# Optimization experiments

Measured on AMD Instinct MI355X. Metric: run time of the kernel, lower is better.

The kernel has to match this reference:

```python
import jax, jax.numpy as jnp
import numpy as np

B, C, H, W = 4, 2048, 14, 14
N_CLS, WORD_D, INT_D = 80, 300, 1024


def setup_inputs() -> dict:
    key = jax.random.key(0)
    ks = jax.random.split(key, 8)
    s = lambda fan_in: 1.0 / np.sqrt(fan_in)
    return {
        "img_feature_map": jax.random.normal(ks[0], (B, C, H, W), jnp.float32),
        "word_features": jax.random.normal(ks[1], (N_CLS, WORD_D), jnp.float32),
        "fc1_w": jax.random.uniform(ks[2], (INT_D, C), jnp.float32, -s(C), s(C)),
        "fc2_w": jax.random.uniform(ks[3], (INT_D, WORD_D), jnp.float32, -s(WORD_D), s(WORD_D)),
        "fc3_w": jax.random.uniform(ks[4], (INT_D, INT_D), jnp.float32, -s(INT_D), s(INT_D)),
        "fc3_b": jax.random.uniform(ks[5], (INT_D,), jnp.float32, -s(INT_D), s(INT_D)),
        "fc4_w": jax.random.uniform(ks[6], (1, INT_D), jnp.float32, -s(INT_D), s(INT_D)),
        "fc4_b": jax.random.uniform(ks[7], (1,), jnp.float32, -s(INT_D), s(INT_D)),
    }


def reference(img_feature_map, word_features, fc1_w, fc2_w, fc3_w, fc3_b, fc4_w, fc4_b):
    b, c, h, w = img_feature_map.shape
    n = word_features.shape[0]
    # [B,C,H,W] -> [B,H,W,C]
    x = jnp.transpose(img_feature_map, (0, 2, 3, 1))
    img_p = jnp.einsum('bhwc,dc->bhwd', x, fc1_w)            # [B,H,W,INT_D]
    word_p = word_features @ fc2_w.T                          # [N,INT_D]
    # broadcast product instead of .repeat(): [B,H,W,N,INT_D]
    feat = jnp.tanh(img_p[:, :, :, None, :] * word_p[None, None, None, :, :])
    feat = jnp.einsum('bhwnd,ed->bhwne', feat, fc3_w) + fc3_b
    coef = jnp.einsum('bhwnd,d->bhwn', feat, fc4_w[0]) + fc4_b[0]  # [B,H,W,N]
    # softmax over spatial positions per (batch, class)
    coef = jax.nn.softmax(coef.reshape(b, h * w, n), axis=1).reshape(b, h, w, n)
    # weighted spatial pooling: [B,N,C]
    return jnp.einsum('bhwn,bhwc->bnc', coef, x)
```

## Files before the change

kernel.cpp:

```cpp
#include <hip/hip_runtime.h>

typedef __attribute__((ext_vector_type(8))) short short8;
typedef __attribute__((ext_vector_type(4))) float f32x4;
typedef __attribute__((ext_vector_type(4))) unsigned short u16x4;

#define B_   4
#define C_   2048
#define HW_  196
#define P_   784
#define NCLS 80
#define WD   300
#define ID   1024

#define WP_OFF    0
#define V_OFF     81920
#define BS_OFF    82944
#define IMGP_OFF  83968
#define LG_OFF    3295232
#define VPART_OFF 3357952
#define ABF_BYTE  13748224
#define WBF_BYTE  16959488

__device__ __forceinline__ unsigned short f2bf(float x) {
    unsigned u = __float_as_uint(x);
    return (unsigned short)((u + 0x7FFFu + ((u >> 16) & 1u)) >> 16);
}

__global__ __launch_bounds__(256) void k_prep(const float* __restrict__ img,
                                              const float* __restrict__ wf,
                                              const float* __restrict__ fc1w,
                                              const float* __restrict__ fc2w,
                                              const float* __restrict__ fc3w,
                                              const float* __restrict__ fc4w,
                                              unsigned short* __restrict__ abf,
                                              unsigned short* __restrict__ wbf,
                                              float* __restrict__ wp,
                                              float* __restrict__ vpart) {
    __shared__ unsigned short tile[HW_][68];
    int bid = blockIdx.x, t = threadIdx.x;
    if (bid < 320) {
        int idx = bid * 256 + t;
        int n = idx >> 10, d = idx & 1023;
        const float4* a = (const float4*)(wf + n * WD);
        const float4* b = (const float4*)(fc2w + d * WD);
        float s = 0.f;
        #pragma unroll 5
        for (int k = 0; k < WD / 4; ++k) {
            float4 x = a[k], y = b[k];
            s += x.x * y.x + x.y * y.y + x.z * y.z + x.w * y.w;
        }
        wp[idx] = s;
    } else if (bid < 832) {
        size_t base = (size_t)(bid - 320) * 4096 + (size_t)t * 16;
        #pragma unroll
        for (int j = 0; j < 4; ++j) {
            float4 v4 = *(const float4*)(fc1w + base + j * 4);
            u16x4 r = {f2bf(v4.x), f2bf(v4.y), f2bf(v4.z), f2bf(v4.w)};
            *(u16x4*)(wbf + base + j * 4) = r;
        }
    } else if (bid < 960) {
        int bc = bid - 832;
        int c0 = (bc >> 2) * 64, b = bc & 3;
        for (int idx = t; idx < 64 * HW_; idx += 256) {
            int c = idx / HW_, hw = idx - c * HW_;
            tile[hw][c] = f2bf(img[((size_t)b * C_ + c0 + c) * HW_ + hw]);
        }
        __syncthreads();
        for (int q = t; q < 16 * HW_; q += 256) {
            int hw = q >> 4, c4 = (q & 15) * 4;
            u16x4 r = *(const u16x4*)&tile[hw][c4];
            *(u16x4*)(abf + ((size_t)b * HW_ + hw) * C_ + c0 + c4) = r;
        }
    } else {
        int idx = bid - 960;
        int ec = idx >> 2;
        int d = (idx & 3) * 256 + t;
        float s = 0.f;
        #pragma unroll 8
        for (int e = ec * 64; e < ec * 64 + 64; ++e) s += fc4w[e] * fc3w[e * ID + d];
        vpart[ec * ID + d] = s;
    }
}

#define LDT 72
__global__ __launch_bounds__(256) void k_fc1(const unsigned short* __restrict__ Abf,
                                             const unsigned short* __restrict__ Wbf,
                                             const float* __restrict__ fc3b,
                                             const float* __restrict__ fc4w,
                                             const float* __restrict__ fc4b,
                                             const float* __restrict__ vpart,
                                             float* __restrict__ imgp4,
                                             float* __restrict__ v,
                                             float* __restrict__ bs) {
    __shared__ unsigned short As[2][64 * LDT];
    __shared__ unsigned short Bs[2][64 * LDT];
    int t = threadIdx.x;
    int bx = blockIdx.x, by = blockIdx.y, bz = blockIdx.z;
    int w = t >> 6, l = t & 63;
    int lr = l & 15, lhi = l >> 4;
    int row = t >> 2, cq = (t & 3) * 16;

    int pA = bx * 64 + row;
    int pAc = pA < P_ ? pA : P_ - 1;
    const unsigned short* aBase = Abf + (size_t)pAc * C_ + bz * 512 + cq;
    const unsigned short* bBase = Wbf + (size_t)(by * 64 + row) * C_ + bz * 512 + cq;

    short8 ra0, ra1, rb0, rb1;
    f32x4 acc[4];
    #pragma unroll
    for (int j = 0; j < 4; ++j) acc[j] = (f32x4){0.f, 0.f, 0.f, 0.f};

    #define LOADR(kc) { \
        const short8* ap = (const short8*)(aBase + (kc) * 64); \
        const short8* bp = (const short8*)(bBase + (kc) * 64); \
        ra0 = ap[0]; ra1 = ap[1]; rb0 = bp[0]; rb1 = bp[1]; }
    #define WRITES(buf) { \
        *(short8*)&As[buf][row * LDT + cq]     = ra0; \
        *(short8*)&As[buf][row * LDT + cq + 8] = ra1; \
        *(short8*)&Bs[buf][row * LDT + cq]     = rb0; \
        *(short8*)&Bs[buf][row * LDT + cq + 8] = rb1; }

    LOADR(0);
    WRITES(0);
    __syncthreads();

    for (int kc = 0; kc < 8; ++kc) {
        int cur = kc & 1;
        if (kc < 7) LOADR(kc + 1);
        #pragma unroll
        for (int kk = 0; kk < 2; ++kk) {
            short8 af = *reinterpret_cast<const short8*>(
                &As[cur][(w * 16 + lr) * LDT + kk * 32 + lhi * 8]);
            #pragma unroll
            for (int j = 0; j < 4; ++j) {
                short8 bfr = *reinterpret_cast<const short8*>(
                    &Bs[cur][(j * 16 + lr) * LDT + kk * 32 + lhi * 8]);
                acc[j] = __builtin_amdgcn_mfma_f32_16x16x32_bf16(af, bfr, acc[j], 0, 0, 0);
            }
        }
        if (kc < 7) WRITES(cur ^ 1);
        __syncthreads();
    }
    #undef LOADR
    #undef WRITES

    float* outp = imgp4 + (size_t)bz * (P_ * ID);
    int prow = bx * 64 + w * 16 + lhi * 4;
    int dcol = by * 64 + lr;
    #pragma unroll
    for (int j = 0; j < 4; ++j)
        #pragma unroll
        for (int i = 0; i < 4; ++i)
            if (prow + i < P_) outp[(size_t)(prow + i) * ID + dcol + j * 16] = acc[j][i];

    if (bx == 0 && by == 0 && bz == 0) {
        for (int d = t; d < ID; d += 256) {
            float s = 0.f;
            #pragma unroll
            for (int k = 0; k < 16; ++k) s += vpart[k * ID + d];
            v[d] = s;
        }
        float s = 0.f;
        for (int i = t; i < ID; i += 256) s += fc3b[i] * fc4w[i];
        __syncthreads();
        float* red = (float*)&As[0][0];
        red[t] = s; __syncthreads();
        for (int o = 128; o > 0; o >>= 1) { if (t < o) red[t] += red[t + o]; __syncthreads(); }
        if (t == 0) bs[0] = red[0] + fc4b[0];
    }
}

__global__ __launch_bounds__(256) void k_logits(const float* __restrict__ imgp4,
                                                const float* __restrict__ wp,
                                                const float* __restrict__ v,
                                                const float* __restrict__ bs,
                                                float* __restrict__ lg) {
    __shared__ float wpl[8 * ID];
    int bx = blockIdx.x, by = blockIdx.y;
    int t = threadIdx.x, wv = t >> 6, lane = t & 63;
    int p = bx * 4 + wv;
    const int S = P_ * ID;
    const float* ap = imgp4 + (size_t)p * ID;
    const float K2 = 2.8853900817779268f;
    f32x4 a2[4], nv2[4];
    float sv = 0.f;
    #pragma unroll
    for (int q = 0; q < 4; ++q) {
        int d = q * 256 + lane * 4;
        f32x4 aq = *(const f32x4*)(ap + d);
        aq += *(const f32x4*)(ap + S + d);
        aq += *(const f32x4*)(ap + 2 * S + d);
        aq += *(const f32x4*)(ap + 3 * S + d);
        f32x4 vq = *(const f32x4*)(v + d);
        a2[q] = aq * K2;
        nv2[q] = vq * -2.0f;
        sv += vq.x + vq.y + vq.z + vq.w;
    }
    float bsv = bs[0];
    int n0 = by * 40;
    for (int ch = 0; ch < 5; ++ch) {
        __syncthreads();
        #pragma unroll
        for (int j = 0; j < 8; ++j) {
            int flat = t * 32 + j * 4;
            *(f32x4*)(wpl + flat) =
                *(const f32x4*)(wp + (size_t)(n0 + ch * 8 + (flat >> 10)) * ID + (flat & 1023));
        }
        __syncthreads();
        #pragma unroll
        for (int r = 0; r < 8; ++r) {
            float s = sv;
            #pragma unroll
            for (int q = 0; q < 4; ++q) {
                f32x4 wq = *(const f32x4*)(wpl + r * ID + q * 256 + lane * 4);
                float e0 = __builtin_amdgcn_exp2f(a2[q].x * wq.x);
                float e1 = __builtin_amdgcn_exp2f(a2[q].y * wq.y);
                float e2 = __builtin_amdgcn_exp2f(a2[q].z * wq.z);
                float e3 = __builtin_amdgcn_exp2f(a2[q].w * wq.w);
                s += nv2[q].x * __builtin_amdgcn_rcpf(e0 + 1.f);
                s += nv2[q].y * __builtin_amdgcn_rcpf(e1 + 1.f);
                s += nv2[q].z * __builtin_amdgcn_rcpf(e2 + 1.f);
                s += nv2[q].w * __builtin_amdgcn_rcpf(e3 + 1.f);
            }
            #pragma unroll
            for (int off = 32; off > 0; off >>= 1) s += __shfl_xor(s, off, 64);
            if (lane == 0) lg[p * NCLS + n0 + ch * 8 + r] = s + bsv;
        }
    }
}

__global__ __launch_bounds__(256) void k_pool(const float* __restrict__ lg,
                                              const float* __restrict__ img,
                                              float* __restrict__ out) {
    __shared__ float smt[16 * HW_];
    int cb = blockIdx.x, nt = blockIdx.y, b = blockIdx.z, t = threadIdx.x;
    int n_l = t >> 4, seg = t & 15;
    int n = nt * 16 + n_l;
    float xr[13];
    float mx = -1e30f;
    #pragma unroll
    for (int j = 0; j < 13; ++j) {
        int hw = seg + j * 16;
        float x = (hw < HW_) ? lg[(size_t)(b * HW_ + hw) * NCLS + n] : -1e30f;
        xr[j] = x; mx = fmaxf(mx, x);
    }
    #pragma unroll
    for (int o = 8; o > 0; o >>= 1) mx = fmaxf(mx, __shfl_xor(mx, o, 16));
    float sum = 0.f;
    #pragma unroll
    for (int j = 0; j < 13; ++j) {
        int hw = seg + j * 16;
        float e = (hw < HW_) ? __expf(xr[j] - mx) : 0.f;
        xr[j] = e; sum += e;
    }
    #pragma unroll
    for (int o = 8; o > 0; o >>= 1) sum += __shfl_xor(sum, o, 16);
    float inv = __builtin_amdgcn_rcpf(sum);
    #pragma unroll
    for (int j = 0; j < 13; ++j) {
        int hw = seg + j * 16;
        if (hw < HW_) smt[n_l * HW_ + hw] = xr[j] * inv;
    }
    __syncthreads();

    int c = cb * 256 + t;
    const float* row = img + ((size_t)b * C_ + c) * HW_;
    float acc[16] = {};
    for (int h4 = 0; h4 < HW_ / 4; ++h4) {
        float4 iv = *(const float4*)(row + h4 * 4);
        #pragma unroll
        for (int nl = 0; nl < 16; ++nl) {
            float4 s4 = *(const float4*)&smt[nl * HW_ + h4 * 4];
            acc[nl] += iv.x * s4.x + iv.y * s4.y + iv.z * s4.z + iv.w * s4.w;
        }
    }
    #pragma unroll
    for (int nl = 0; nl < 16; ++nl)
        out[((size_t)b * NCLS + nt * 16 + nl) * C_ + c] = acc[nl];
}

extern "C" void kernel_launch(void* const* d_in, const int* in_sizes, int n_in,
                              void* d_out, int out_size, void* d_ws, size_t ws_size,
                              hipStream_t stream) {
    const float* img  = (const float*)d_in[0];
    const float* wf   = (const float*)d_in[1];
    const float* fc1w = (const float*)d_in[2];
    const float* fc2w = (const float*)d_in[3];
    const float* fc3w = (const float*)d_in[4];
    const float* fc3b = (const float*)d_in[5];
    const float* fc4w = (const float*)d_in[6];
    const float* fc4b = (const float*)d_in[7];
    float* out = (float*)d_out;
    float* ws  = (float*)d_ws;

    float* wp    = ws + WP_OFF;
    float* v     = ws + V_OFF;
    float* bs    = ws + BS_OFF;
    float* imgp4 = ws + IMGP_OFF;
    float* lg    = ws + LG_OFF;
    float* vpart = ws + VPART_OFF;
    unsigned short* Abf = (unsigned short*)((char*)d_ws + ABF_BYTE);
    unsigned short* Wbf = (unsigned short*)((char*)d_ws + WBF_BYTE);

    k_prep   <<<dim3(1024),      256, 0, stream>>>(img, wf, fc1w, fc2w, fc3w, fc4w,
                                                   Abf, Wbf, wp, vpart);
    k_fc1    <<<dim3(13, 16, 4), 256, 0, stream>>>(Abf, Wbf, fc3b, fc4w, fc4b, vpart,
                                                   imgp4, v, bs);
    k_logits <<<dim3(196, 2),    256, 0, stream>>>(imgp4, wp, v, bs, lg);
    k_pool   <<<dim3(8, 5, 4),   256, 0, stream>>>(lg, img, out);
}
```

Before: 169.5 us.

## Drop LDS staging in fc1 GEMM, split logits grid, separate softmax kernel

The fc1 bf16 MFMA GEMM no longer double-buffers tiles through shared memory. Each lane now loads its MFMA fragments straight from global memory, which removes the LDS writes and barriers but makes the B-operand reads redundant across the four waves. The logits kernel is split over four class groups of 20 instead of two of 40, doubling the block count, with 10-row shared tiles. Softmax moves out of the pooling kernel into its own kernel that writes normalized weights to workspace, and pooling reads them from global memory instead of LDS. This costs one extra launch and a round trip through memory.

Result: slower. 189.8 us (+12.0%).

```diff
diff --git a/kernel.cpp b/kernel.cpp
--- a/kernel.cpp
+++ b/kernel.cpp
@@ -18,6 +18,7 @@
 #define IMGP_OFF  83968
 #define LG_OFF    3295232
 #define VPART_OFF 3357952
+#define SM_OFF    3374336
 #define ABF_BYTE  13748224
 #define WBF_BYTE  16959488
 
@@ -82,7 +83,6 @@
     }
 }
 
-#define LDT 72
 __global__ __launch_bounds__(256) void k_fc1(const unsigned short* __restrict__ Abf,
                                              const unsigned short* __restrict__ Wbf,
                                              const float* __restrict__ fc3b,
@@ -92,57 +92,30 @@
                                              float* __restrict__ imgp4,
                                              float* __restrict__ v,
                                              float* __restrict__ bs) {
-    __shared__ unsigned short As[2][64 * LDT];
-    __shared__ unsigned short Bs[2][64 * LDT];
+    __shared__ float red[256];
     int t = threadIdx.x;
     int bx = blockIdx.x, by = blockIdx.y, bz = blockIdx.z;
     int w = t >> 6, l = t & 63;
     int lr = l & 15, lhi = l >> 4;
-    int row = t >> 2, cq = (t & 3) * 16;
-
-    int pA = bx * 64 + row;
+
+    int pA = bx * 64 + w * 16 + lr;
     int pAc = pA < P_ ? pA : P_ - 1;
-    const unsigned short* aBase = Abf + (size_t)pAc * C_ + bz * 512 + cq;
-    const unsigned short* bBase = Wbf + (size_t)(by * 64 + row) * C_ + bz * 512 + cq;
-
-    short8 ra0, ra1, rb0, rb1;
+    const unsigned short* aBase = Abf + (size_t)pAc * C_ + bz * 512 + lhi * 8;
+    const unsigned short* bBase = Wbf + (size_t)(by * 64 + lr) * C_ + bz * 512 + lhi * 8;
+
     f32x4 acc[4];
     #pragma unroll
     for (int j = 0; j < 4; ++j) acc[j] = (f32x4){0.f, 0.f, 0.f, 0.f};
 
-    #define LOADR(kc) { \
-        const short8* ap = (const short8*)(aBase + (kc) * 64); \
-        const short8* bp = (const short8*)(bBase + (kc) * 64); \
-        ra0 = ap[0]; ra1 = ap[1]; rb0 = bp[0]; rb1 = bp[1]; }
-    #define WRITES(buf) { \
-        *(short8*)&As[buf][row * LDT + cq]     = ra0; \
-        *(short8*)&As[buf][row * LDT + cq + 8] = ra1; \
-        *(short8*)&Bs[buf][row * LDT + cq]     = rb0; \
-        *(short8*)&Bs[buf][row * LDT + cq + 8] = rb1; }
-
-    LOADR(0);
-    WRITES(0);
-    __syncthreads();
-
-    for (int kc = 0; kc < 8; ++kc) {
-        int cur = kc & 1;
-        if (kc < 7) LOADR(kc + 1);
-        #pragma unroll
-        for (int kk = 0; kk < 2; ++kk) {
-            short8 af = *reinterpret_cast<const short8*>(
-                &As[cur][(w * 16 + lr) * LDT + kk * 32 + lhi * 8]);
-            #pragma unroll
-            for (int j = 0; j < 4; ++j) {
-                short8 bfr = *reinterpret_cast<const short8*>(
-                    &Bs[cur][(j * 16 + lr) * LDT + kk * 32 + lhi * 8]);
-                acc[j] = __builtin_amdgcn_mfma_f32_16x16x32_bf16(af, bfr, acc[j], 0, 0, 0);
-            }
-        }
-        if (kc < 7) WRITES(cur ^ 1);
-        __syncthreads();
-    }
-    #undef LOADR
-    #undef WRITES
+    #pragma unroll 4
+    for (int k2 = 0; k2 < 16; ++k2) {
+        short8 af = *(const short8*)(aBase + k2 * 32);
+        #pragma unroll
+        for (int j = 0; j < 4; ++j) {
+            short8 bf = *(const short8*)(bBase + (size_t)j * 16 * C_ + k2 * 32);
+            acc[j] = __builtin_amdgcn_mfma_f32_16x16x32_bf16(af, bf, acc[j], 0, 0, 0);
+        }
+    }
 
     float* outp = imgp4 + (size_t)bz * (P_ * ID);
     int prow = bx * 64 + w * 16 + lhi * 4;
@@ -162,8 +135,6 @@
         }
         float s = 0.f;
         for (int i = t; i < ID; i += 256) s += fc3b[i] * fc4w[i];
-        __syncthreads();
-        float* red = (float*)&As[0][0];
         red[t] = s; __syncthreads();
         for (int o = 128; o > 0; o >>= 1) { if (t < o) red[t] += red[t + o]; __syncthreads(); }
         if (t == 0) bs[0] = red[0] + fc4b[0];
@@ -175,7 +146,7 @@
                                                 const float* __restrict__ v,
                                                 const float* __restrict__ bs,
                                                 float* __restrict__ lg) {
-    __shared__ float wpl[8 * ID];
+    __shared__ float wpl[10 * ID];
     int bx = blockIdx.x, by = blockIdx.y;
     int t = threadIdx.x, wv = t >> 6, lane = t & 63;
     int p = bx * 4 + wv;
@@ -197,18 +168,19 @@
         sv += vq.x + vq.y + vq.z + vq.w;
     }
     float bsv = bs[0];
-    int n0 = by * 40;
-    for (int ch = 0; ch < 5; ++ch) {
+    int n0 = by * 20;
+    #pragma unroll
+    for (int ch = 0; ch < 2; ++ch) {
         __syncthreads();
         #pragma unroll
-        for (int j = 0; j < 8; ++j) {
-            int flat = t * 32 + j * 4;
+        for (int j = 0; j < 10; ++j) {
+            int flat = t * 40 + j * 4;
             *(f32x4*)(wpl + flat) =
-                *(const f32x4*)(wp + (size_t)(n0 + ch * 8 + (flat >> 10)) * ID + (flat & 1023));
+                *(const f32x4*)(wp + (size_t)(n0 + ch * 10 + (flat >> 10)) * ID + (flat & 1023));
         }
         __syncthreads();
-        #pragma unroll
-        for (int r = 0; r < 8; ++r) {
+        #pragma unroll 2
+        for (int r = 0; r < 10; ++r) {
             float s = sv;
             #pragma unroll
             for (int q = 0; q < 4; ++q) {
@@ -224,53 +196,39 @@
             }
             #pragma unroll
             for (int off = 32; off > 0; off >>= 1) s += __shfl_xor(s, off, 64);
-            if (lane == 0) lg[p * NCLS + n0 + ch * 8 + r] = s + bsv;
-        }
-    }
-}
-
-__global__ __launch_bounds__(256) void k_pool(const float* __restrict__ lg,
+            if (lane == 0) lg[p * NCLS + n0 + ch * 10 + r] = s + bsv;
+        }
+    }
+}
+
+__global__ __launch_bounds__(256) void k_softmax(const float* __restrict__ lg,
+                                                 float* __restrict__ sm) {
+    __shared__ float red[256];
+    int b = blockIdx.x, n = blockIdx.y, t = threadIdx.x;
+    float x = (t < HW_) ? lg[(size_t)(b * HW_ + t) * NCLS + n] : -1e30f;
+    red[t] = x; __syncthreads();
+    for (int o = 128; o > 0; o >>= 1) { if (t < o) red[t] = fmaxf(red[t], red[t + o]); __syncthreads(); }
+    float mx = red[0]; __syncthreads();
+    float e = (t < HW_) ? __expf(x - mx) : 0.f;
+    red[t] = e; __syncthreads();
+    for (int o = 128; o > 0; o >>= 1) { if (t < o) red[t] += red[t + o]; __syncthreads(); }
+    float inv = __builtin_amdgcn_rcpf(red[0]);
+    if (t < HW_) sm[((size_t)b * NCLS + n) * HW_ + t] = e * inv;
+}
+
+__global__ __launch_bounds__(256) void k_pool(const float* __restrict__ sm,
                                               const float* __restrict__ img,
                                               float* __restrict__ out) {
-    __shared__ float smt[16 * HW_];
     int cb = blockIdx.x, nt = blockIdx.y, b = blockIdx.z, t = threadIdx.x;
-    int n_l = t >> 4, seg = t & 15;
-    int n = nt * 16 + n_l;
-    float xr[13];
-    float mx = -1e30f;
-    #pragma unroll
-    for (int j = 0; j < 13; ++j) {
-        int hw = seg + j * 16;
-        float x = (hw < HW_) ? lg[(size_t)(b * HW_ + hw) * NCLS + n] : -1e30f;
-        xr[j] = x; mx = fmaxf(mx, x);
-    }
-    #pragma unroll
-    for (int o = 8; o > 0; o >>= 1) mx = fmaxf(mx, __shfl_xor(mx, o, 16));
-    float sum = 0.f;
-    #pragma unroll
-    for (int j = 0; j < 13; ++j) {
-        int hw = seg + j * 16;
-        float e = (hw < HW_) ? __expf(xr[j] - mx) : 0.f;
-        xr[j] = e; sum += e;
-    }
-    #pragma unroll
-    for (int o = 8; o > 0; o >>= 1) sum += __shfl_xor(sum, o, 16);
-    float inv = __builtin_amdgcn_rcpf(sum);
-    #pragma unroll
-    for (int j = 0; j < 13; ++j) {
-        int hw = seg + j * 16;
-        if (hw < HW_) smt[n_l * HW_ + hw] = xr[j] * inv;
-    }
-    __syncthreads();
-
     int c = cb * 256 + t;
     const float* row = img + ((size_t)b * C_ + c) * HW_;
+    const float* smb = sm + ((size_t)b * NCLS + nt * 16) * HW_;
     float acc[16] = {};
     for (int h4 = 0; h4 < HW_ / 4; ++h4) {
         float4 iv = *(const float4*)(row + h4 * 4);
         #pragma unroll
         for (int nl = 0; nl < 16; ++nl) {
-            float4 s4 = *(const float4*)&smt[nl * HW_ + h4 * 4];
+            float4 s4 = *(const float4*)(smb + nl * HW_ + h4 * 4);
             acc[nl] += iv.x * s4.x + iv.y * s4.y + iv.z * s4.z + iv.w * s4.w;
         }
     }
@@ -299,6 +257,7 @@
     float* imgp4 = ws + IMGP_OFF;
     float* lg    = ws + LG_OFF;
     float* vpart = ws + VPART_OFF;
+    float* sm    = ws + SM_OFF;
     unsigned short* Abf = (unsigned short*)((char*)d_ws + ABF_BYTE);
     unsigned short* Wbf = (unsigned short*)((char*)d_ws + WBF_BYTE);
 
@@ -306,6 +265,7 @@
                                                    Abf, Wbf, wp, vpart);
     k_fc1    <<<dim3(13, 16, 4), 256, 0, stream>>>(Abf, Wbf, fc3b, fc4w, fc4b, vpart,
                                                    imgp4, v, bs);
-    k_logits <<<dim3(196, 2),    256, 0, stream>>>(imgp4, wp, v, bs, lg);
-    k_pool   <<<dim3(8, 5, 4),   256, 0, stream>>>(lg, img, out);
-}
+    k_logits <<<dim3(196, 4),    256, 0, stream>>>(imgp4, wp, v, bs, lg);
+    k_softmax<<<dim3(4, 80),     256, 0, stream>>>(lg, sm);
+    k_pool   <<<dim3(8, 5, 4),   256, 0, stream>>>(sm, img, out);
+}
```
